# Kernel optimization log

Measured on AMD Instinct MI355X. Metric: run time of the kernel, lower is better.

## Reference

```python
import jax, jax.numpy as jnp
import numpy as np

TEMPERATURE = 0.1


def _l2norm(x):
    return x / jnp.linalg.norm(x, axis=1, keepdims=True)


def _unif(x, t=2.0):
    # torch.pdist(x).pow(2) == squared euclidean distances over pairs i<j
    m = x.shape[0]
    sq = jnp.sum(x * x, axis=1)
    d2 = sq[:, None] + sq[None, :] - 2.0 * (x @ x.T)  # [m, m]
    d2 = jnp.maximum(d2, 0.0)
    iu = jnp.triu(jnp.ones((m, m), dtype=bool), k=1)
    s = jnp.sum(jnp.where(iu, jnp.exp(-t * d2), 0.0))
    n_pairs = m * (m - 1) // 2
    return jnp.log(s / n_pairs)


def setup_inputs() -> dict:
    key = jax.random.key(0)
    k1, k2 = jax.random.split(key)
    proj_1 = jax.random.normal(k1, (4096, 1024), dtype=jnp.float32)
    proj_2 = jax.random.normal(k2, (4096, 1024), dtype=jnp.float32)
    return {"proj_1": proj_1, "proj_2": proj_2}


def reference(proj_1, proj_2):
    n = proj_1.shape[0]
    t = TEMPERATURE
    z_i = _l2norm(proj_1)
    z_j = _l2norm(proj_2)
    z = jnp.concatenate([z_i, z_j], axis=0)  # [2n, d]
    # rows are unit-norm, so cosine similarity == dot product
    sim = z @ z.T  # [2n, 2n]
    # diag(sim, +n) == diag(sim, -n) == rowwise z_i . z_j
    pos = jnp.sum(z_i * z_j, axis=1)  # [n]
    positives = jnp.concatenate([pos, pos], axis=0)  # [2n]
    mask = 1.0 - jnp.eye(2 * n, dtype=sim.dtype)
    denom = jnp.sum(mask * jnp.exp(sim / t), axis=1)  # [2n]
    # -log(exp(pos/t) / denom) == log(denom) - pos/t
    loss = jnp.sum(jnp.log(denom) - positives / t) / (2 * n)
    # alignment: mean ||z_i - z_j||_2^2 (alpha=2), detached
    lalign = jax.lax.stop_gradient(jnp.mean(jnp.sum((z_i - z_j) ** 2, axis=1)))
    # uniformity on the two halves of z_i, detached
    lunif = jax.lax.stop_gradient(
        (_unif(z_i[: n // 2]) + _unif(z_i[n // 2 :])) / 2.0
    )
    return (loss, lalign, lunif)
```

## Files before the change

### kernel.cpp

```cpp
#include <hip/hip_runtime.h>
#include <stdint.h>

#define DDIM   1024
#define M_TOT  8192
#define N_ROWS 4096
#define KT     16
#define NCELL  2080
#define SLOT   16384
#define NSLOT  3
#define LDS_TOTAL (NSLOT * SLOT)

typedef __attribute__((ext_vector_type(4))) float f32x4;
typedef __attribute__((ext_vector_type(2))) long i64x2;

__device__ __forceinline__ void gload_lds16(const void* g, void* l) {
  __builtin_amdgcn_global_load_lds(
      (const __attribute__((address_space(1))) uint32_t*)g,
      (__attribute__((address_space(3))) uint32_t*)l, 16, 0, 0);
}

__global__ __launch_bounds__(256) void knorm(const float* __restrict__ p1,
                                             const float* __restrict__ p2,
                                             unsigned char* __restrict__ z8,
                                             float* __restrict__ pp,
                                             float* __restrict__ ap,
                                             float* __restrict__ denom,
                                             float* __restrict__ uacc) {
  const int r = blockIdx.x;
  const int t = threadIdx.x;
  const int lane = t & 63, w = t >> 6;
  __shared__ float red0[4], red1[4];

  if (t < 2) denom[r * 2 + t] = 0.0f;
  if (r < 64 && t < 2) uacc[t * 64 + r] = 0.0f;

  const float4 a = ((const float4*)(p1 + (size_t)r * DDIM))[t];
  const float4 b = ((const float4*)(p2 + (size_t)r * DDIM))[t];
  float s1 = a.x*a.x + a.y*a.y + a.z*a.z + a.w*a.w;
  float s2 = b.x*b.x + b.y*b.y + b.z*b.z + b.w*b.w;
  for (int off = 1; off < 64; off <<= 1) { s1 += __shfl_xor(s1, off); s2 += __shfl_xor(s2, off); }
  if (lane == 0) { red0[w] = s1; red1[w] = s2; }
  __syncthreads();
  const float S1 = red0[0] + red0[1] + red0[2] + red0[3];
  const float S2 = red1[0] + red1[1] + red1[2] + red1[3];
  const float r1 = 1.0f / sqrtf(S1);
  const float r2 = 1.0f / sqrtf(S2);
  const float n1x = a.x*r1, n1y = a.y*r1, n1z = a.z*r1, n1w = a.w*r1;
  const float n2x = b.x*r2, n2y = b.y*r2, n2z = b.z*r2, n2w = b.w*r2;
  float pos = n1x*n2x + n1y*n2y + n1z*n2z + n1w*n2w;
  float al  = (n1x-n2x)*(n1x-n2x) + (n1y-n2y)*(n1y-n2y)
            + (n1z-n2z)*(n1z-n2z) + (n1w-n2w)*(n1w-n2w);
  __syncthreads();
  for (int off = 1; off < 64; off <<= 1) { pos += __shfl_xor(pos, off); al += __shfl_xor(al, off); }
  if (lane == 0) { red0[w] = pos; red1[w] = al; }
  __syncthreads();
  if (t == 0) {
    pp[r] = red0[0] + red0[1] + red0[2] + red0[3];
    ap[r] = red1[0] + red1[1] + red1[2] + red1[3];
  }
  const int g = t >> 4, c = (t >> 1) & 7, h = t & 1;
  const int sp = (c < 4) ? (2 * c) : (2 * (c - 4) + 1);
  const int off = g * 64 + sp * 8 + h * 4;
  int w1 = __builtin_amdgcn_cvt_pk_fp8_f32(n1x, n1y, 0, false);
  w1     = __builtin_amdgcn_cvt_pk_fp8_f32(n1z, n1w, w1, true);
  int w2 = __builtin_amdgcn_cvt_pk_fp8_f32(n2x, n2y, 0, false);
  w2     = __builtin_amdgcn_cvt_pk_fp8_f32(n2z, n2w, w2, true);
  *(int*)(z8 + (size_t)r * 1024 + off) = w1;
  *(int*)(z8 + (size_t)(r + N_ROWS) * 1024 + off) = w2;
}

__device__ __forceinline__ void stage64(const char* zb, int rowA0, int colB0,
                                        int kt, char* slot, int wid, int lane) {
  const int kb = kt * 64 + (lane >> 4) * 16;
  const int rowin = lane & 15;
  const int u0 = wid * 2, u1 = wid * 2 + 1;
  gload_lds16(zb + (size_t)(rowA0 + u0 * 16 + rowin) * 1024 + kb, slot + u0 * 1024 + lane * 16);
  gload_lds16(zb + (size_t)(rowA0 + u1 * 16 + rowin) * 1024 + kb, slot + u1 * 1024 + lane * 16);
  gload_lds16(zb + (size_t)(colB0 + u0 * 16 + rowin) * 1024 + kb, slot + 8192 + u0 * 1024 + lane * 16);
  gload_lds16(zb + (size_t)(colB0 + u1 * 16 + rowin) * 1024 + kb, slot + 8192 + u1 * 1024 + lane * 16);
}

__global__ __launch_bounds__(256, 3) void kgemm(const unsigned char* __restrict__ z,
                                                float* __restrict__ denom,
                                                float* __restrict__ uacc) {
  extern __shared__ char lds[];
  const int tid  = threadIdx.x;
  const int lane = tid & 63, wid = tid >> 6;
  const int wsr  = wid >> 1, wsc = wid & 1;
  const int lr = lane >> 4, lc = lane & 15;
  const char* zb = (const char*)z;
  const float RK10 = 14.426950408889634f;
  const float K4   = 5.770780163555856f;

  const int cdx = (blockIdx.x & 7) * 260 + (blockIdx.x >> 3);
  int SI = (int)((sqrtf(16.0f + 128.0f * (float)cdx) - 4.0f) * (1.0f / 64.0f));
  while (32 * (SI + 1) * (SI + 1) + 4 * (SI + 1) <= cdx) ++SI;
  while (32 * SI * SI + 4 * SI > cdx) --SI;
  int rem = cdx - (32 * SI * SI + 4 * SI);
  int I, J;
  if (rem < 36) {
    int ii = (int)((sqrtf(8.0f * (float)rem + 1.0f) - 1.0f) * 0.5f);
    while ((ii + 1) * (ii + 2) / 2 <= rem) ++ii;
    while (ii * (ii + 1) / 2 > rem) --ii;
    const int jj = rem - ii * (ii + 1) / 2;
    I = SI * 8 + ii; J = SI * 8 + jj;
  } else {
    const int r2 = rem - 36;
    const int SJ = r2 >> 6, w = r2 & 63;
    I = SI * 8 + (w >> 3); J = SJ * 8 + (w & 7);
  }
  const int rowA0 = I * 128, colB0 = J * 128;
  const bool useful = (colB0 + wsc * 64) < (rowA0 + wsr * 64 + 64);

  f32x4 acc[4][4] = {};

  stage64(zb, rowA0, colB0, 0, lds, wid, lane);
  stage64(zb, rowA0, colB0, 1, lds + SLOT, wid, lane);
  asm volatile("s_waitcnt vmcnt(4)" ::: "memory");
  __builtin_amdgcn_s_barrier();
  __builtin_amdgcn_sched_barrier(0);

#pragma unroll 1
  for (int t = 0; t < KT; ++t) {
    if (t + 2 < KT)
      stage64(zb, rowA0, colB0, t + 2, lds + ((t + 2) % 3) * SLOT, wid, lane);
    __builtin_amdgcn_sched_barrier(0);
    const char* S = lds + (t % 3) * SLOT;
    if (useful) {
      const char* Ab = S + wsr * 4096 + lr * 256 + lc * 16;
      const char* Bb = S + 8192 + wsc * 4096 + lr * 256 + lc * 16;
      i64x2 af[4], bg[4];
#pragma unroll
      for (int m = 0; m < 4; ++m) {
        af[m] = *(const i64x2*)(Ab + m * 1024);
        bg[m] = *(const i64x2*)(Bb + m * 1024);
      }
      __builtin_amdgcn_s_setprio(1);
#pragma unroll
      for (int q = 0; q < 2; ++q)
#pragma unroll
        for (int m = 0; m < 4; ++m)
#pragma unroll
          for (int n = 0; n < 4; ++n)
            acc[m][n] = __builtin_amdgcn_mfma_f32_16x16x32_fp8_fp8(
                af[m][q], bg[n][q], acc[m][n], 0, 0, 0);
      __builtin_amdgcn_s_setprio(0);
    }
    if (t + 2 < KT) asm volatile("s_waitcnt vmcnt(4)" ::: "memory");
    else            asm volatile("s_waitcnt vmcnt(0)" ::: "memory");
    __builtin_amdgcn_s_barrier();
    __builtin_amdgcn_sched_barrier(0);
  }

  const bool unif = (I < 16) || (I < 32 && J >= 16);
  if (useful) {
    float cs[4] = {0.0f, 0.0f, 0.0f, 0.0f};
    float u = 0.0f;
#pragma unroll
    for (int m = 0; m < 4; ++m) {
      const int growb = rowA0 + wsr * 64 + m * 16 + lr * 4;
#pragma unroll
      for (int i = 0; i < 4; ++i) {
        const int grow = growb + i;
        float rs = 0.0f;
#pragma unroll
        for (int n = 0; n < 4; ++n) {
          const int gcol = colB0 + wsc * 64 + n * 16 + lc;
          const bool incl = (gcol < grow);
          float e = incl ? exp2f(acc[m][n][i] * RK10) : 0.0f;
          rs += e;
          cs[n] += e;
          if (unif) u += incl ? exp2f(acc[m][n][i] * K4 - K4) : 0.0f;
        }
        rs += __shfl_xor(rs, 1); rs += __shfl_xor(rs, 2);
        rs += __shfl_xor(rs, 4); rs += __shfl_xor(rs, 8);
        if (lc == 0 && rs > 0.0f) atomicAdd(&denom[grow], rs);
      }
    }
#pragma unroll
    for (int n = 0; n < 4; ++n) {
      float cv = cs[n];
      cv += __shfl_xor(cv, 16); cv += __shfl_xor(cv, 32);
      if (lr == 0 && cv > 0.0f) atomicAdd(&denom[colB0 + wsc * 64 + n * 16 + lc], cv);
    }
    if (unif) {
      for (int off = 1; off < 64; off <<= 1) u += __shfl_xor(u, off);
      if (lane == 0 && u > 0.0f)
        atomicAdd(&uacc[((I < 16) ? 0 : 64) + (blockIdx.x & 63)], 2.0f * u);
    }
  }
}

__global__ __launch_bounds__(1024) void klogf(const float* __restrict__ denom,
                                              const float* __restrict__ pp,
                                              const float* __restrict__ ap,
                                              const float* __restrict__ uacc,
                                              float* __restrict__ out) {
  __shared__ float redl[16], redp[16], reda[16], ured[2];
  const int tid = threadIdx.x;
  float s = 0.0f, sp = 0.0f, sa = 0.0f;
#pragma unroll
  for (int q = 0; q < 8; ++q) s += logf(denom[q * 1024 + tid]);
#pragma unroll
  for (int q = 0; q < 4; ++q) { sp += pp[q * 1024 + tid]; sa += ap[q * 1024 + tid]; }
  const int lane = tid & 63, w = tid >> 6;
  for (int off = 1; off < 64; off <<= 1) {
    s += __shfl_xor(s, off); sp += __shfl_xor(sp, off); sa += __shfl_xor(sa, off);
  }
  if (lane == 0) { redl[w] = s; redp[w] = sp; reda[w] = sa; }
  if (tid < 64) {
    float u0 = uacc[tid], u1 = uacc[64 + tid];
    for (int off = 1; off < 64; off <<= 1) { u0 += __shfl_xor(u0, off); u1 += __shfl_xor(u1, off); }
    if (tid == 0) { ured[0] = u0; ured[1] = u1; }
  }
  __syncthreads();
  if (tid == 0) {
    float S = 0.0f, SP = 0.0f, SA = 0.0f;
#pragma unroll
    for (int i = 0; i < 16; ++i) { S += redl[i]; SP += redp[i]; SA += reda[i]; }
    const float P = 2048.0f * 2047.0f * 0.5f;
    out[0] = (S - 20.0f * SP) / 8192.0f;
    out[1] = SA / 4096.0f;
    out[2] = 0.5f * (logf(ured[0] * 0.5f / P) + logf(ured[1] * 0.5f / P));
  }
}

extern "C" void kernel_launch(void* const* d_in, const int* in_sizes, int n_in,
                              void* d_out, int out_size, void* d_ws, size_t ws_size,
                              hipStream_t stream) {
  const float* p1 = (const float*)d_in[0];
  const float* p2 = (const float*)d_in[1];
  float* out = (float*)d_out;
  char* ws = (char*)d_ws;
  unsigned char* z8 = (unsigned char*)ws;
  float* denom = (float*)(ws + (size_t)M_TOT * DDIM);
  float* uacc  = denom + M_TOT;
  float* pp    = uacc + 128;
  float* ap    = pp + 4096;

  (void)hipFuncSetAttribute((const void*)kgemm,
                            hipFuncAttributeMaxDynamicSharedMemorySize, LDS_TOTAL);
  knorm<<<N_ROWS, 256, 0, stream>>>(p1, p2, z8, pp, ap, denom, uacc);
  kgemm<<<NCELL, 256, LDS_TOTAL, stream>>>(z8, denom, uacc);
  klogf<<<1, 1024, 0, stream>>>(denom, pp, ap, uacc, out);
}
```

Before: 92.39 us.

## Split GEMM tiles into single-wave 64x64 quadrant blocks with early exit

Each 128x128 triangular cell is split into four independent 64-lane blocks, each computing one 64x64 quadrant with its own double-buffered LDS staging. Quadrants entirely above the diagonal now return early rather than idling through the K loop, and block-wide barriers disappear. In exchange, A/B tiles are no longer shared across the waves of a cell, so global/L2 traffic per cell roughly doubles, and the pipeline drops from triple to double buffering.

```diff
diff --git a/kernel.cpp b/kernel.cpp
--- a/kernel.cpp
+++ b/kernel.cpp
@@ -5,10 +5,9 @@
 #define M_TOT  8192
 #define N_ROWS 4096
 #define KT     16
-#define NCELL  2080
-#define SLOT   16384
-#define NSLOT  3
-#define LDS_TOTAL (NSLOT * SLOT)
+#define NQUAD  8320
+#define SLOTW  8192
+#define LDS_TOTAL (2 * SLOTW)
 
 typedef __attribute__((ext_vector_type(4))) float f32x4;
 typedef __attribute__((ext_vector_type(2))) long i64x2;
@@ -69,34 +68,37 @@
   *(int*)(z8 + (size_t)(r + N_ROWS) * 1024 + off) = w2;
 }
 
-__device__ __forceinline__ void stage64(const char* zb, int rowA0, int colB0,
-                                        int kt, char* slot, int wid, int lane) {
+__device__ __forceinline__ void stageW(const char* zb, int arow0, int bcol0,
+                                       int kt, char* slot, int lane) {
   const int kb = kt * 64 + (lane >> 4) * 16;
   const int rowin = lane & 15;
-  const int u0 = wid * 2, u1 = wid * 2 + 1;
-  gload_lds16(zb + (size_t)(rowA0 + u0 * 16 + rowin) * 1024 + kb, slot + u0 * 1024 + lane * 16);
-  gload_lds16(zb + (size_t)(rowA0 + u1 * 16 + rowin) * 1024 + kb, slot + u1 * 1024 + lane * 16);
-  gload_lds16(zb + (size_t)(colB0 + u0 * 16 + rowin) * 1024 + kb, slot + 8192 + u0 * 1024 + lane * 16);
-  gload_lds16(zb + (size_t)(colB0 + u1 * 16 + rowin) * 1024 + kb, slot + 8192 + u1 * 1024 + lane * 16);
-}
-
-__global__ __launch_bounds__(256, 3) void kgemm(const unsigned char* __restrict__ z,
-                                                float* __restrict__ denom,
-                                                float* __restrict__ uacc) {
+#pragma unroll
+  for (int u = 0; u < 4; ++u)
+    gload_lds16(zb + (size_t)(arow0 + u * 16 + rowin) * 1024 + kb,
+                slot + u * 1024 + lane * 16);
+#pragma unroll
+  for (int u = 0; u < 4; ++u)
+    gload_lds16(zb + (size_t)(bcol0 + u * 16 + rowin) * 1024 + kb,
+                slot + 4096 + u * 1024 + lane * 16);
+}
+
+__global__ __launch_bounds__(64) void kgemm(const unsigned char* __restrict__ z,
+                                            float* __restrict__ denom,
+                                            float* __restrict__ uacc) {
   extern __shared__ char lds[];
-  const int tid  = threadIdx.x;
-  const int lane = tid & 63, wid = tid >> 6;
-  const int wsr  = wid >> 1, wsc = wid & 1;
+  const int lane = threadIdx.x & 63;
   const int lr = lane >> 4, lc = lane & 15;
   const char* zb = (const char*)z;
   const float RK10 = 14.426950408889634f;
   const float K4   = 5.770780163555856f;
 
-  const int cdx = (blockIdx.x & 7) * 260 + (blockIdx.x >> 3);
-  int SI = (int)((sqrtf(16.0f + 128.0f * (float)cdx) - 4.0f) * (1.0f / 64.0f));
-  while (32 * (SI + 1) * (SI + 1) + 4 * (SI + 1) <= cdx) ++SI;
-  while (32 * SI * SI + 4 * SI > cdx) --SI;
-  int rem = cdx - (32 * SI * SI + 4 * SI);
+  const int cq = (blockIdx.x & 7) * 1040 + (blockIdx.x >> 3);
+  const int cell = cq >> 2, quad = cq & 3;
+  const int wsr = quad >> 1, wsc = quad & 1;
+  int SI = (int)((sqrtf(16.0f + 128.0f * (float)cell) - 4.0f) * (1.0f / 64.0f));
+  while (32 * (SI + 1) * (SI + 1) + 4 * (SI + 1) <= cell) ++SI;
+  while (32 * SI * SI + 4 * SI > cell) --SI;
+  int rem = cell - (32 * SI * SI + 4 * SI);
   int I, J;
   if (rem < 36) {
     int ii = (int)((sqrtf(8.0f * (float)rem + 1.0f) - 1.0f) * 0.5f);
@@ -110,84 +112,80 @@
     I = SI * 8 + (w >> 3); J = SJ * 8 + (w & 7);
   }
   const int rowA0 = I * 128, colB0 = J * 128;
-  const bool useful = (colB0 + wsc * 64) < (rowA0 + wsr * 64 + 64);
+  const int arow0 = rowA0 + wsr * 64, bcol0 = colB0 + wsc * 64;
+  if (bcol0 >= arow0 + 64) return;
 
   f32x4 acc[4][4] = {};
 
-  stage64(zb, rowA0, colB0, 0, lds, wid, lane);
-  stage64(zb, rowA0, colB0, 1, lds + SLOT, wid, lane);
-  asm volatile("s_waitcnt vmcnt(4)" ::: "memory");
-  __builtin_amdgcn_s_barrier();
-  __builtin_amdgcn_sched_barrier(0);
+  stageW(zb, arow0, bcol0, 0, lds, lane);
+  stageW(zb, arow0, bcol0, 1, lds + SLOTW, lane);
+  asm volatile("s_waitcnt vmcnt(8)" ::: "memory");
 
 #pragma unroll 1
   for (int t = 0; t < KT; ++t) {
-    if (t + 2 < KT)
-      stage64(zb, rowA0, colB0, t + 2, lds + ((t + 2) % 3) * SLOT, wid, lane);
-    __builtin_amdgcn_sched_barrier(0);
-    const char* S = lds + (t % 3) * SLOT;
-    if (useful) {
-      const char* Ab = S + wsr * 4096 + lr * 256 + lc * 16;
-      const char* Bb = S + 8192 + wsc * 4096 + lr * 256 + lc * 16;
-      i64x2 af[4], bg[4];
-#pragma unroll
-      for (int m = 0; m < 4; ++m) {
-        af[m] = *(const i64x2*)(Ab + m * 1024);
-        bg[m] = *(const i64x2*)(Bb + m * 1024);
+    char* S = lds + (t & 1) * SLOTW;
+    const char* Ab = S + lr * 256 + lc * 16;
+    const char* Bb = S + 4096 + lr * 256 + lc * 16;
+    i64x2 af[4], bg[4];
+#pragma unroll
+    for (int m = 0; m < 4; ++m) {
+      af[m] = *(const i64x2*)(Ab + m * 1024);
+      bg[m] = *(const i64x2*)(Bb + m * 1024);
+    }
+    __builtin_amdgcn_s_setprio(1);
+#pragma unroll
+    for (int q = 0; q < 2; ++q)
+#pragma unroll
+      for (int m = 0; m < 4; ++m)
+#pragma unroll
+        for (int n = 0; n < 4; ++n)
+          acc[m][n] = __builtin_amdgcn_mfma_f32_16x16x32_fp8_fp8(
+              af[m][q], bg[n][q], acc[m][n], 0, 0, 0);
+    __builtin_amdgcn_s_setprio(0);
+    if (t + 2 < KT) {
+      asm volatile("s_waitcnt lgkmcnt(0)" ::: "memory");
+      __builtin_amdgcn_sched_barrier(0);
+      stageW(zb, arow0, bcol0, t + 2, S, lane);
+      asm volatile("s_waitcnt vmcnt(8)" ::: "memory");
+    } else if (t + 1 < KT) {
+      asm volatile("s_waitcnt vmcnt(0)" ::: "memory");
+    }
+  }
+
+  const bool unif = (I < 16) || (I < 32 && J >= 16);
+  float cs[4] = {0.0f, 0.0f, 0.0f, 0.0f};
+  float u = 0.0f;
+#pragma unroll
+  for (int m = 0; m < 4; ++m) {
+    const int growb = arow0 + m * 16 + lr * 4;
+#pragma unroll
+    for (int i = 0; i < 4; ++i) {
+      const int grow = growb + i;
+      float rs = 0.0f;
+#pragma unroll
+      for (int n = 0; n < 4; ++n) {
+        const int gcol = bcol0 + n * 16 + lc;
+        const bool incl = (gcol < grow);
+        float e = incl ? exp2f(acc[m][n][i] * RK10) : 0.0f;
+        rs += e;
+        cs[n] += e;
+        if (unif) u += incl ? exp2f(acc[m][n][i] * K4 - K4) : 0.0f;
       }
-      __builtin_amdgcn_s_setprio(1);
-#pragma unroll
-      for (int q = 0; q < 2; ++q)
-#pragma unroll
-        for (int m = 0; m < 4; ++m)
-#pragma unroll
-          for (int n = 0; n < 4; ++n)
-            acc[m][n] = __builtin_amdgcn_mfma_f32_16x16x32_fp8_fp8(
-                af[m][q], bg[n][q], acc[m][n], 0, 0, 0);
-      __builtin_amdgcn_s_setprio(0);
+      rs += __shfl_xor(rs, 1); rs += __shfl_xor(rs, 2);
+      rs += __shfl_xor(rs, 4); rs += __shfl_xor(rs, 8);
+      if (lc == 0 && rs > 0.0f) atomicAdd(&denom[grow], rs);
     }
-    if (t + 2 < KT) asm volatile("s_waitcnt vmcnt(4)" ::: "memory");
-    else            asm volatile("s_waitcnt vmcnt(0)" ::: "memory");
-    __builtin_amdgcn_s_barrier();
-    __builtin_amdgcn_sched_barrier(0);
-  }
-
-  const bool unif = (I < 16) || (I < 32 && J >= 16);
-  if (useful) {
-    float cs[4] = {0.0f, 0.0f, 0.0f, 0.0f};
-    float u = 0.0f;
-#pragma unroll
-    for (int m = 0; m < 4; ++m) {
-      const int growb = rowA0 + wsr * 64 + m * 16 + lr * 4;
-#pragma unroll
-      for (int i = 0; i < 4; ++i) {
-        const int grow = growb + i;
-        float rs = 0.0f;
-#pragma unroll
-        for (int n = 0; n < 4; ++n) {
-          const int gcol = colB0 + wsc * 64 + n * 16 + lc;
-          const bool incl = (gcol < grow);
-          float e = incl ? exp2f(acc[m][n][i] * RK10) : 0.0f;
-          rs += e;
-          cs[n] += e;
-          if (unif) u += incl ? exp2f(acc[m][n][i] * K4 - K4) : 0.0f;
-        }
-        rs += __shfl_xor(rs, 1); rs += __shfl_xor(rs, 2);
-        rs += __shfl_xor(rs, 4); rs += __shfl_xor(rs, 8);
-        if (lc == 0 && rs > 0.0f) atomicAdd(&denom[grow], rs);
-      }
-    }
-#pragma unroll
-    for (int n = 0; n < 4; ++n) {
-      float cv = cs[n];
-      cv += __shfl_xor(cv, 16); cv += __shfl_xor(cv, 32);
-      if (lr == 0 && cv > 0.0f) atomicAdd(&denom[colB0 + wsc * 64 + n * 16 + lc], cv);
-    }
-    if (unif) {
-      for (int off = 1; off < 64; off <<= 1) u += __shfl_xor(u, off);
-      if (lane == 0 && u > 0.0f)
-        atomicAdd(&uacc[((I < 16) ? 0 : 64) + (blockIdx.x & 63)], 2.0f * u);
-    }
+  }
+#pragma unroll
+  for (int n = 0; n < 4; ++n) {
+    float cv = cs[n];
+    cv += __shfl_xor(cv, 16); cv += __shfl_xor(cv, 32);
+    if (lr == 0 && cv > 0.0f) atomicAdd(&denom[bcol0 + n * 16 + lc], cv);
+  }
+  if (unif) {
+    for (int off = 1; off < 64; off <<= 1) u += __shfl_xor(u, off);
+    if (lane == 0 && u > 0.0f)
+      atomicAdd(&uacc[((I < 16) ? 0 : 64) + (blockIdx.x & 63)], 2.0f * u);
   }
 }
 
@@ -241,6 +239,6 @@
   (void)hipFuncSetAttribute((const void*)kgemm,
                             hipFuncAttributeMaxDynamicSharedMemorySize, LDS_TOTAL);
   knorm<<<N_ROWS, 256, 0, stream>>>(p1, p2, z8, pp, ap, denom, uacc);
-  kgemm<<<NCELL, 256, LDS_TOTAL, stream>>>(z8, denom, uacc);
+  kgemm<<<NQUAD, 64, LDS_TOTAL, stream>>>(z8, denom, uacc);
   klogf<<<1, 1024, 0, stream>>>(denom, pp, ap, uacc, out);
 }
```

Result: slower. 144.0 us (+55.9%).
